# Kernel optimization log

Hardware: AMD Instinct MI355X
Metric: run time of the kernel (lower is better)

## Reference

```python
import jax, jax.numpy as jnp
import numpy as np

LN_EPS = 1e-5

def _layernorm(x, w, b):
    mu = jnp.mean(x, axis=-1, keepdims=True)
    var = jnp.mean(jnp.square(x - mu), axis=-1, keepdims=True)
    return (x - mu) * jax.lax.rsqrt(var + LN_EPS) * w + b

def setup_inputs() -> dict:
    key = jax.random.key(0)
    ks = jax.random.split(key, 8)
    B, T, D, E = 8, 4096, 1024, 4
    inner = 4 * D
    x = jax.random.normal(ks[0], (B, T, D), dtype=jnp.float32)
    router_prob = jax.random.uniform(ks[1], (B, T, E), dtype=jnp.float32)
    alpha = jnp.ones((), dtype=jnp.float32)
    norm_w = jnp.ones((D,), dtype=jnp.float32)
    norm_b = jnp.zeros((D,), dtype=jnp.float32)
    l1_w = jax.random.normal(ks[2], (inner, D), dtype=jnp.float32) * 0.02
    l1_b = jax.random.normal(ks[3], (inner,), dtype=jnp.float32) * 0.02
    l2_w = jax.random.normal(ks[4], (D, inner), dtype=jnp.float32) * 0.02
    l2_b = jax.random.normal(ks[5], (D,), dtype=jnp.float32) * 0.02
    return {"x": x, "router_prob": router_prob, "alpha": alpha,
            "norm_w": norm_w, "norm_b": norm_b,
            "l1_w": l1_w, "l1_b": l1_b, "l2_w": l2_w, "l2_b": l2_b}

def reference(x, router_prob, alpha, norm_w, norm_b, l1_w, l1_b, l2_w, l2_b):
    B, T, D = x.shape
    E = router_prob.shape[2]
    n = T // E  # tokens per expert (contiguous slices)
    outs = []
    for e in range(E):  # small fixed loop; each expert has a different width m
        xs = x[:, e * n:(e + 1) * n, :]              # [B,n,D]
        h = _layernorm(xs, norm_w, norm_b)
        m = D // (2 ** e)                             # Matryoshka width
        he = h[:, :, :m]                              # [B,n,m]
        # dropout is a no-op in eval mode
        inner = jax.nn.gelu(jnp.einsum('btm,im->bti', he, l1_w[:, :m]) + l1_b,
                            approximate=False)        # [B,n,4D]
        out = jnp.einsum('bti,mi->btm', inner, l2_w[:m, :]) + l2_b[:m]  # [B,n,m]
        out = jnp.pad(out, ((0, 0), (0, 0), (0, D - m)))
        scale = alpha * router_prob[:, e * n:(e + 1) * n, e] + 1.0      # [B,n]
        outs.append(xs + scale[:, :, None] * out)
    return jnp.concatenate(outs, axis=1)
```

## Files before the change

kernel.cpp:

```cpp
#include <hip/hip_runtime.h>
#include <cstdint>

#define DD     1024
#define NINNER 4096
#define NTOK   32768
#define MROWS  8192

typedef unsigned short u16;
typedef __bf16 bf16x8 __attribute__((ext_vector_type(8)));
typedef float  f32x4  __attribute__((ext_vector_type(4)));

__device__ __forceinline__ u16 f2bf(float f) {
    union { float f; uint32_t u; } a; a.f = f;
    uint32_t r = a.u + 0x7fffu + ((a.u >> 16) & 1u);
    return (u16)(r >> 16);
}

__device__ __forceinline__ void async16(const void* g, void* l) {
    __builtin_amdgcn_global_load_lds(
        (const __attribute__((address_space(1))) void*)g,
        (__attribute__((address_space(3))) void*)l,
        16, 0, 0);
}

__global__ __launch_bounds__(256) void cast_w(
    const float* __restrict__ w1, const float* __restrict__ w2,
    u16* __restrict__ w1b, u16* __restrict__ w2b)
{
    int idx = blockIdx.x * 256 + threadIdx.x;
    const int n1 = (NINNER * DD) / 4;
    float4 v; ushort4 o;
    if (idx < n1) {
        v = ((const float4*)w1)[idx];
        o.x = f2bf(v.x); o.y = f2bf(v.y); o.z = f2bf(v.z); o.w = f2bf(v.w);
        ((ushort4*)w1b)[idx] = o;
    } else {
        int j = idx - n1;
        v = ((const float4*)w2)[j];
        o.x = f2bf(v.x); o.y = f2bf(v.y); o.z = f2bf(v.z); o.w = f2bf(v.w);
        ((ushort4*)w2b)[j] = o;
    }
}

__global__ __launch_bounds__(256) void ln_kernel(
    const float* __restrict__ x, const float* __restrict__ nw,
    const float* __restrict__ nb, u16* __restrict__ h,
    float* __restrict__ out)
{
    const int row = blockIdx.x;
    const int tid = threadIdx.x;
    const float4 v = ((const float4*)(x + (size_t)row * DD))[tid];
    float s  = v.x + v.y + v.z + v.w;
    float s2 = v.x*v.x + v.y*v.y + v.z*v.z + v.w*v.w;
#pragma unroll
    for (int o = 32; o > 0; o >>= 1) {
        s  += __shfl_down(s,  o, 64);
        s2 += __shfl_down(s2, o, 64);
    }
    __shared__ float as1[4], as2[4];
    if ((tid & 63) == 0) { as1[tid >> 6] = s; as2[tid >> 6] = s2; }
    __syncthreads();
    const float S  = as1[0] + as1[1] + as1[2] + as1[3];
    const float S2 = as2[0] + as2[1] + as2[2] + as2[3];
    const float mu  = S  * (1.0f / 1024.0f);
    const float var = S2 * (1.0f / 1024.0f) - mu * mu;
    const float rs  = rsqrtf(var + 1e-5f);
    const float4 w4 = ((const float4*)nw)[tid];
    const float4 b4 = ((const float4*)nb)[tid];
    ushort4 hv;
    hv.x = f2bf((v.x - mu) * rs * w4.x + b4.x);
    hv.y = f2bf((v.y - mu) * rs * w4.y + b4.y);
    hv.z = f2bf((v.z - mu) * rs * w4.z + b4.z);
    hv.w = f2bf((v.w - mu) * rs * w4.w + b4.w);
    ((ushort4*)(h + (size_t)row * DD))[tid] = hv;
    const int e = (row >> 10) & 3;
    const int m = DD >> e;
    if (tid * 4 >= m)
        ((float4*)(out + (size_t)row * DD))[tid] = v;
}


__global__ __launch_bounds__(256) void gemm1(
    const u16* __restrict__ h, const u16* __restrict__ w1b,
    const float* __restrict__ l1b, u16* __restrict__ inner,
    int K, int e)
{
    __shared__ u16 lA[128 * 64];
    __shared__ u16 lB[128 * 64];
    const int tid  = threadIdx.x;
    const int lane = tid & 63;
    const int w    = tid >> 6;
    const int wr   = w >> 1, wc = w & 1;
    const int bm = blockIdx.y, bn = blockIdx.x;

    f32x4 acc[4][4] = {};

    const int srow = (lane >> 3);
    const int soff = ((lane & 7) ^ srow) * 8;

    for (int kt = 0; kt < K; kt += 64) {
#pragma unroll
        for (int i = 0; i < 4; ++i) {
            const int c   = w * 4 + i;
            const int row = c * 8 + srow;
            const int rl  = bm * 128 + row;
            const int g   = ((rl >> 10) << 12) + (e << 10) + (rl & 1023);
            async16(h + (size_t)g * DD + kt + soff, &lA[c * 512]);
        }
#pragma unroll
        for (int i = 0; i < 4; ++i) {
            const int c   = w * 4 + i;
            const int row = c * 8 + srow;
            async16(w1b + (size_t)(bn * 128 + row) * DD + kt + soff, &lB[c * 512]);
        }
        __syncthreads();
#pragma unroll
        for (int kk = 0; kk < 2; ++kk) {
            const int sg = ((kk * 4 + (lane >> 4)) ^ (lane & 7)) * 8;
            bf16x8 af[4], bq[4];
#pragma unroll
            for (int i = 0; i < 4; ++i)
                af[i] = *(const bf16x8*)&lA[(wr * 64 + i * 16 + (lane & 15)) * 64 + sg];
#pragma unroll
            for (int i = 0; i < 4; ++i)
                bq[i] = *(const bf16x8*)&lB[(wc * 64 + i * 16 + (lane & 15)) * 64 + sg];
#pragma unroll
            for (int mi = 0; mi < 4; ++mi)
#pragma unroll
                for (int ni = 0; ni < 4; ++ni)
                    acc[mi][ni] = __builtin_amdgcn_mfma_f32_16x16x32_bf16(
                        af[mi], bq[ni], acc[mi][ni], 0, 0, 0);
        }
        __syncthreads();
    }

    const int cbase = bn * 128 + wc * 64 + (lane & 15);
    const int rbase = bm * 128 + wr * 64 + (lane >> 4) * 4;
#pragma unroll
    for (int ni = 0; ni < 4; ++ni) {
        const int col = cbase + ni * 16;
        const float bias = l1b[col];
#pragma unroll
        for (int mi = 0; mi < 4; ++mi) {
            const int r0 = rbase + mi * 16;
#pragma unroll
            for (int r = 0; r < 4; ++r) {
                const float vv = acc[mi][ni][r] + bias;
                const float gg = 0.5f * vv * (1.0f + erff(vv * 0.7071067811865476f));
                inner[(size_t)(r0 + r) * NINNER + col] = f2bf(gg);
            }
        }
    }
}

__global__ __launch_bounds__(256) void gemm2(
    const u16* __restrict__ inner, const u16* __restrict__ w2b,
    const float* __restrict__ l2b, const float* __restrict__ x,
    const float* __restrict__ rp, const float* __restrict__ alphap,
    float* __restrict__ out, int e)
{
    __shared__ u16 lA[128 * 64];
    __shared__ u16 lB[128 * 64];
    const int tid  = threadIdx.x;
    const int lane = tid & 63;
    const int w    = tid >> 6;
    const int wr   = w >> 1, wc = w & 1;
    const int bm = blockIdx.y, bn = blockIdx.x;

    f32x4 acc[4][4] = {};
    const int srow = (lane >> 3);
    const int soff = ((lane & 7) ^ srow) * 8;

    for (int kt = 0; kt < 4096; kt += 64) {
#pragma unroll
        for (int i = 0; i < 4; ++i) {
            const int c   = w * 4 + i;
            const int row = c * 8 + srow;
            async16(inner + (size_t)(bm * 128 + row) * NINNER + kt + soff, &lA[c * 512]);
        }
#pragma unroll
        for (int i = 0; i < 4; ++i) {
            const int c   = w * 4 + i;
            const int row = c * 8 + srow;
            async16(w2b + (size_t)(bn * 128 + row) * NINNER + kt + soff, &lB[c * 512]);
        }
        __syncthreads();
#pragma unroll
        for (int kk = 0; kk < 2; ++kk) {
            const int sg = ((kk * 4 + (lane >> 4)) ^ (lane & 7)) * 8;
            bf16x8 af[4], bq[4];
#pragma unroll
            for (int i = 0; i < 4; ++i)
                af[i] = *(const bf16x8*)&lA[(wr * 64 + i * 16 + (lane & 15)) * 64 + sg];
#pragma unroll
            for (int i = 0; i < 4; ++i)
                bq[i] = *(const bf16x8*)&lB[(wc * 64 + i * 16 + (lane & 15)) * 64 + sg];
#pragma unroll
            for (int mi = 0; mi < 4; ++mi)
#pragma unroll
                for (int ni = 0; ni < 4; ++ni)
                    acc[mi][ni] = __builtin_amdgcn_mfma_f32_16x16x32_bf16(
                        af[mi], bq[ni], acc[mi][ni], 0, 0, 0);
        }
        __syncthreads();
    }

    const float alpha = alphap[0];
    const int cbase = bn * 128 + wc * 64 + (lane & 15);
    const int rbase = bm * 128 + wr * 64 + (lane >> 4) * 4;
#pragma unroll
    for (int mi = 0; mi < 4; ++mi) {
#pragma unroll
        for (int r = 0; r < 4; ++r) {
            const int rl = rbase + mi * 16 + r;
            const int g  = ((rl >> 10) << 12) + (e << 10) + (rl & 1023);
            const float sc = alpha * rp[(size_t)g * 4 + e] + 1.0f;
#pragma unroll
            for (int ni = 0; ni < 4; ++ni) {
                const int col = cbase + ni * 16;
                const float v = acc[mi][ni][r] + l2b[col];
                out[(size_t)g * DD + col] = x[(size_t)g * DD + col] + sc * v;
            }
        }
    }
}

extern "C" void kernel_launch(void* const* d_in, const int* in_sizes, int n_in,
                              void* d_out, int out_size, void* d_ws, size_t ws_size,
                              hipStream_t stream) {
    const float* x     = (const float*)d_in[0];
    const float* rp    = (const float*)d_in[1];
    const float* alpha = (const float*)d_in[2];
    const float* nw    = (const float*)d_in[3];
    const float* nb    = (const float*)d_in[4];
    const float* l1w   = (const float*)d_in[5];
    const float* l1b   = (const float*)d_in[6];
    const float* l2w   = (const float*)d_in[7];
    const float* l2b   = (const float*)d_in[8];
    float* out = (float*)d_out;

    char* ws = (char*)d_ws;
    if (ws_size < ((size_t)144 << 20)) return;
    u16* h     = (u16*)(ws);
    u16* inner = (u16*)(ws + ((size_t)64 << 20));
    u16* w1b   = (u16*)(ws + ((size_t)128 << 20));
    u16* w2b   = (u16*)(ws + ((size_t)136 << 20));

    cast_w<<<8192, 256, 0, stream>>>(l1w, l2w, w1b, w2b);
    ln_kernel<<<NTOK, 256, 0, stream>>>(x, nw, nb, h, out);
    for (int e = 0; e < 4; ++e) {
        const int m = DD >> e;
        gemm1<<<dim3(NINNER / 128, MROWS / 128), 256, 0, stream>>>(h, w1b, l1b, inner, m, e);
        gemm2<<<dim3(m / 128, MROWS / 128), 256, 0, stream>>>(inner, w2b, l2b, x, rp, alpha, out, e);
    }
}
```

Measured before the change: 870.1 us.

## Split-K gemm2 with atomic accumulation and XCD-aware block mapping

New measurement: 864.4 us. Within noise of the previous version (-0.7%).

```diff
diff --git a/kernel.cpp b/kernel.cpp
--- a/kernel.cpp
+++ b/kernel.cpp
@@ -44,8 +44,9 @@
 
 __global__ __launch_bounds__(256) void ln_kernel(
     const float* __restrict__ x, const float* __restrict__ nw,
-    const float* __restrict__ nb, u16* __restrict__ h,
-    float* __restrict__ out)
+    const float* __restrict__ nb, const float* __restrict__ l2b,
+    const float* __restrict__ rp, const float* __restrict__ alphap,
+    u16* __restrict__ h, float* __restrict__ out)
 {
     const int row = blockIdx.x;
     const int tid = threadIdx.x;
@@ -73,10 +74,19 @@
     hv.z = f2bf((v.z - mu) * rs * w4.z + b4.z);
     hv.w = f2bf((v.w - mu) * rs * w4.w + b4.w);
     ((ushort4*)(h + (size_t)row * DD))[tid] = hv;
+
     const int e = (row >> 10) & 3;
     const int m = DD >> e;
-    if (tid * 4 >= m)
-        ((float4*)(out + (size_t)row * DD))[tid] = v;
+    float4 o4;
+    if (tid * 4 < m) {
+        const float sc = alphap[0] * rp[(size_t)row * 4 + e] + 1.0f;
+        const float4 lb = ((const float4*)l2b)[tid];
+        o4.x = v.x + sc * lb.x; o4.y = v.y + sc * lb.y;
+        o4.z = v.z + sc * lb.z; o4.w = v.w + sc * lb.w;
+    } else {
+        o4 = v;
+    }
+    ((float4*)(out + (size_t)row * DD))[tid] = o4;
 }
 
 
@@ -155,9 +165,8 @@
 
 __global__ __launch_bounds__(256) void gemm2(
     const u16* __restrict__ inner, const u16* __restrict__ w2b,
-    const float* __restrict__ l2b, const float* __restrict__ x,
     const float* __restrict__ rp, const float* __restrict__ alphap,
-    float* __restrict__ out, int e)
+    float* __restrict__ out, int e, int lgBn, int lgCPB)
 {
     __shared__ u16 lA[128 * 64];
     __shared__ u16 lB[128 * 64];
@@ -165,13 +174,22 @@
     const int lane = tid & 63;
     const int w    = tid >> 6;
     const int wr   = w >> 1, wc = w & 1;
-    const int bm = blockIdx.y, bn = blockIdx.x;
+
+    const int id    = blockIdx.x;
+    const int xcd   = id & 7;
+    const int j     = id >> 3;
+    const int bm    = ((j >> lgCPB) << 3) | xcd;
+    const int chunk = j & ((1 << lgCPB) - 1);
+    const int bn    = chunk & ((1 << lgBn) - 1);
+    const int s     = chunk >> lgBn;
+    const int Kc    = NINNER >> (lgCPB - lgBn);
+    const int k0    = s * Kc;
 
     f32x4 acc[4][4] = {};
     const int srow = (lane >> 3);
     const int soff = ((lane & 7) ^ srow) * 8;
 
-    for (int kt = 0; kt < 4096; kt += 64) {
+    for (int kt = k0; kt < k0 + Kc; kt += 64) {
 #pragma unroll
         for (int i = 0; i < 4; ++i) {
             const int c   = w * 4 + i;
@@ -218,8 +236,7 @@
 #pragma unroll
             for (int ni = 0; ni < 4; ++ni) {
                 const int col = cbase + ni * 16;
-                const float v = acc[mi][ni][r] + l2b[col];
-                out[(size_t)g * DD + col] = x[(size_t)g * DD + col] + sc * v;
+                unsafeAtomicAdd(out + (size_t)g * DD + col, sc * acc[mi][ni][r]);
             }
         }
     }
@@ -247,10 +264,13 @@
     u16* w2b   = (u16*)(ws + ((size_t)136 << 20));
 
     cast_w<<<8192, 256, 0, stream>>>(l1w, l2w, w1b, w2b);
-    ln_kernel<<<NTOK, 256, 0, stream>>>(x, nw, nb, h, out);
+    ln_kernel<<<NTOK, 256, 0, stream>>>(x, nw, nb, l2b, rp, alpha, h, out);
+    static const int lgBn_t[4]  = {3, 2, 1, 0};
+    static const int lgCPB_t[4] = {4, 4, 4, 3};
     for (int e = 0; e < 4; ++e) {
         const int m = DD >> e;
         gemm1<<<dim3(NINNER / 128, MROWS / 128), 256, 0, stream>>>(h, w1b, l1b, inner, m, e);
-        gemm2<<<dim3(m / 128, MROWS / 128), 256, 0, stream>>>(inner, w2b, l2b, x, rp, alpha, out, e);
-    }
-}
+        gemm2<<<64 << lgCPB_t[e], 256, 0, stream>>>(inner, w2b, rp, alpha, out, e,
+                                                    lgBn_t[e], lgCPB_t[e]);
+    }
+}
```
